# Kernel tuning notes

Hardware: AMD Instinct MI355X
Metric: run time of the kernel (lower is better)

Reference implementation:

```python
import jax, jax.numpy as jnp
import numpy as np

QMIN, QMAX = -128, 127  # int8 range


def _quantize(x, scale, zero_point):
    """Affine quantize float -> int8: clamp(round(x/scale) + zp, -128, 127)."""
    q = jnp.round(x / scale) + zero_point
    return jnp.clip(q, QMIN, QMAX).astype(jnp.int8)


def setup_inputs() -> dict:
    key = jax.random.key(0)
    k1, k2, k3 = jax.random.split(key, 3)
    N, IN, OUT = 8192, 4096, 4096
    inp = jax.random.normal(k1, (N, IN), dtype=jnp.float32)
    # int8 weight table [OUT, IN]
    weight = jax.random.randint(k2, (OUT, IN), QMIN, QMAX + 1, dtype=jnp.int32).astype(jnp.int8)
    # int32 bias [OUT]
    bias = jax.random.randint(k3, (OUT,), -(2 ** 15), 2 ** 15, dtype=jnp.int32)
    return {
        "input": inp,
        "weight": weight,
        "bias": bias,
        "input_scale": 0.02,
        "input_zero_point": 0,
        "output_scale": 4096.0,
        "output_zero_point": 0,
    }


def reference(input, weight, bias, input_scale, input_zero_point, output_scale, output_zero_point):
    # 1) affine quantize input to int8
    q_input = _quantize(input, input_scale, input_zero_point)
    # 2) int32 matmul: F.linear(q_input.int32, weight.int32, bias.int32)
    acc = jnp.matmul(q_input.astype(jnp.int32), weight.astype(jnp.int32).T) + bias  # [N, OUT] int32
    # 3) requantize int32 accumulator to int8 with output scale/zero-point
    q_output = _quantize(acc.astype(jnp.float32), output_scale, output_zero_point)
    return q_output
```

## Files before the change

### kernel.cpp

```cpp
#include <hip/hip_runtime.h>
#include <stdint.h>

typedef int v4i __attribute__((ext_vector_type(4)));
typedef int v16i __attribute__((ext_vector_type(16)));

__device__ __forceinline__ int clamp_i8(int v) {
    return v < -128 ? -128 : (v > 127 ? 127 : v);
}

__device__ __forceinline__ void async_load16(const void* g, void* l) {
    __builtin_amdgcn_global_load_lds(
        (const __attribute__((address_space(1))) void*)g,
        (__attribute__((address_space(3))) void*)l, 16, 0, 0);
}

__global__ void quant_input_kernel(const float* __restrict__ x, int8_t* __restrict__ q,
                                   const float* __restrict__ scale_p,
                                   const int* __restrict__ zp_p, int n4) {
    int t = blockIdx.x * blockDim.x + threadIdx.x;
    if (t >= n4) return;
    const float inv = 1.0f / *scale_p;
    const int zp = *zp_p;
    float4 v = ((const float4*)x)[t];
    int q0 = clamp_i8((int)rintf(v.x * inv) + zp);
    int q1 = clamp_i8((int)rintf(v.y * inv) + zp);
    int q2 = clamp_i8((int)rintf(v.z * inv) + zp);
    int q3 = clamp_i8((int)rintf(v.w * inv) + zp);
    int packed = (q0 & 255) | ((q1 & 255) << 8) | ((q2 & 255) << 16) | ((q3 & 255) << 24);
    ((int*)q)[t] = packed;
}

__global__ void pack_weight_kernel(const int* __restrict__ w, int8_t* __restrict__ q, int n4) {
    int t = blockIdx.x * blockDim.x + threadIdx.x;
    if (t >= n4) return;
    int4 v = ((const int4*)w)[t];
    int packed = (v.x & 255) | ((v.y & 255) << 8) | ((v.z & 255) << 16) | ((v.w & 255) << 24);
    ((int*)q)[t] = packed;
}

#define BM 256
#define BN 128
#define BK 64

__global__ __launch_bounds__(256, 2) void gemm_i8_kernel(
    const int8_t* __restrict__ A, const int8_t* __restrict__ W,
    const int* __restrict__ bias, int* __restrict__ C,
    const float* __restrict__ oscale_p, const int* __restrict__ ozp_p,
    int N, int K, int M) {
    __shared__ int8_t lA[BM * BK];
    __shared__ int8_t lB[BN * BK];

    const int tid = threadIdx.x;
    const int lane = tid & 63;
    const int w = tid >> 6;
    const int wm = w >> 1;
    const int wn = w & 1;

    const int bm = blockIdx.y * BM;
    const int bn = blockIdx.x * BN;

    const int s_sub = lane >> 2;
    const int s_col = (((lane & 3) ^ ((s_sub >> 1) & 3))) * 16;
    const int8_t* gA = A + (int64_t)(bm + w * 64 + s_sub) * K + s_col;
    const int8_t* gB = W + (int64_t)(bn + w * 32 + s_sub) * K + s_col;
    int8_t* lA0 = &lA[w * 4096];
    int8_t* lB0 = &lB[w * 2048];
    const int64_t rs = (int64_t)16 * K;

    const int m0 = lane & 31;
    const int rsw = (m0 >> 1) & 3;
    const int chi = lane >> 5;

    v16i acc[4][2];
#pragma unroll
    for (int i = 0; i < 4; i++)
#pragma unroll
        for (int j = 0; j < 2; j++)
#pragma unroll
            for (int r = 0; r < 16; r++) acc[i][j][r] = 0;

    for (int kt = 0; kt < K; kt += BK) {
        async_load16(gA, lA0);
        async_load16(gA + rs, lA0 + 1024);
        async_load16(gA + 2 * rs, lA0 + 2048);
        async_load16(gA + 3 * rs, lA0 + 3072);
        async_load16(gB, lB0);
        async_load16(gB + rs, lB0 + 1024);
        gA += BK;
        gB += BK;
        __syncthreads();

#pragma unroll
        for (int k0 = 0; k0 < BK; k0 += 32) {
            const int cb = k0 >> 4;
            v4i af[4], bf[2];
#pragma unroll
            for (int ms = 0; ms < 4; ms++)
                af[ms] = *(const v4i*)&lA[(wm * 128 + ms * 32 + m0) * BK +
                                          (((cb + chi) ^ rsw) << 4)];
#pragma unroll
            for (int ns = 0; ns < 2; ns++)
                bf[ns] = *(const v4i*)&lB[(wn * 64 + ns * 32 + m0) * BK +
                                          (((cb + chi) ^ rsw) << 4)];

#pragma unroll
            for (int ms = 0; ms < 4; ms++)
#pragma unroll
                for (int ns = 0; ns < 2; ns++)
                    acc[ms][ns] = __builtin_amdgcn_mfma_i32_32x32x32_i8(
                        af[ms], bf[ns], acc[ms][ns], 0, 0, 0);
        }
        __syncthreads();
    }

    const float inv_os = 1.0f / *oscale_p;
    const int ozp = *ozp_p;
    const int rbase = 4 * (lane >> 5);
#pragma unroll
    for (int ns = 0; ns < 2; ns++) {
        const int gn = bn + wn * 64 + ns * 32 + m0;
        const int bv = bias[gn];
#pragma unroll
        for (int ms = 0; ms < 4; ms++) {
            const int gm0 = bm + wm * 128 + ms * 32 + rbase;
            v16i a = acc[ms][ns];
#pragma unroll
            for (int reg = 0; reg < 16; reg++) {
                const int row = (reg & 3) + 8 * (reg >> 2);
                int v = a[reg] + bv;
                int q = (int)rintf((float)v * inv_os) + ozp;
                q = clamp_i8(q);
                C[(int64_t)(gm0 + row) * M + gn] = q;
            }
        }
    }
}

extern "C" void kernel_launch(void* const* d_in, const int* in_sizes, int n_in,
                              void* d_out, int out_size, void* d_ws, size_t ws_size,
                              hipStream_t stream) {
    const float* x = (const float*)d_in[0];
    const int* wgt = (const int*)d_in[1];
    const int* bias = (const int*)d_in[2];
    const float* in_scale = (const float*)d_in[3];
    const int* in_zp = (const int*)d_in[4];
    const float* out_scale = (const float*)d_in[5];
    const int* out_zp = (const int*)d_in[6];

    const int64_t x_elems = (int64_t)in_sizes[0];
    const int OUT = in_sizes[2];
    const int K = in_sizes[1] / OUT;
    const int N = (int)(x_elems / K);

    int8_t* qA = (int8_t*)d_ws;
    int8_t* qW = qA + x_elems;

    {
        int n4 = (int)(x_elems / 4);
        quant_input_kernel<<<(n4 + 255) / 256, 256, 0, stream>>>(x, qA, in_scale, in_zp, n4);
    }
    {
        int n4 = (int)(((int64_t)OUT * K) / 4);
        pack_weight_kernel<<<(n4 + 255) / 256, 256, 0, stream>>>(wgt, qW, n4);
    }
    dim3 grid(OUT / BN, N / BM);
    gemm_i8_kernel<<<grid, 256, 0, stream>>>(qA, qW, bias, (int*)d_out,
                                             out_scale, out_zp, N, K, OUT);
}
```

Before: 424.5 us.

## Double-buffer LDS tiles in int8 GEMM and widen prepass kernels to 16 elements

The GEMM main loop now keeps two LDS buffers for A and B. It prefetches the next K tile with async global-to-LDS loads while MFMAs run on the current tile, which drops one barrier per iteration. The quantize and weight-pack prepass kernels now handle 16 elements per thread and write 16-byte stores instead of 4-byte ones. Doubling LDS to 48KB per block cuts the headroom for occupancy. The overlap only helps if the wait that the barrier inserts does not serialize the prefetch.

Result: no change. 420.0 us (-1.1%).

```diff
diff --git a/kernel.cpp b/kernel.cpp
--- a/kernel.cpp
+++ b/kernel.cpp
@@ -14,28 +14,38 @@
         (__attribute__((address_space(3))) void*)l, 16, 0, 0);
 }
 
-__global__ void quant_input_kernel(const float* __restrict__ x, int8_t* __restrict__ q,
+__global__ void quant_input_kernel(const float4* __restrict__ x, int4* __restrict__ q,
                                    const float* __restrict__ scale_p,
-                                   const int* __restrict__ zp_p, int n4) {
+                                   const int* __restrict__ zp_p, int n16) {
     int t = blockIdx.x * blockDim.x + threadIdx.x;
-    if (t >= n4) return;
+    if (t >= n16) return;
     const float inv = 1.0f / *scale_p;
     const int zp = *zp_p;
-    float4 v = ((const float4*)x)[t];
-    int q0 = clamp_i8((int)rintf(v.x * inv) + zp);
-    int q1 = clamp_i8((int)rintf(v.y * inv) + zp);
-    int q2 = clamp_i8((int)rintf(v.z * inv) + zp);
-    int q3 = clamp_i8((int)rintf(v.w * inv) + zp);
-    int packed = (q0 & 255) | ((q1 & 255) << 8) | ((q2 & 255) << 16) | ((q3 & 255) << 24);
-    ((int*)q)[t] = packed;
-}
-
-__global__ void pack_weight_kernel(const int* __restrict__ w, int8_t* __restrict__ q, int n4) {
+    int4 out;
+    int* op = (int*)&out;
+#pragma unroll
+    for (int j = 0; j < 4; j++) {
+        float4 v = x[4 * t + j];
+        int q0 = clamp_i8((int)rintf(v.x * inv) + zp);
+        int q1 = clamp_i8((int)rintf(v.y * inv) + zp);
+        int q2 = clamp_i8((int)rintf(v.z * inv) + zp);
+        int q3 = clamp_i8((int)rintf(v.w * inv) + zp);
+        op[j] = (q0 & 255) | ((q1 & 255) << 8) | ((q2 & 255) << 16) | ((q3 & 255) << 24);
+    }
+    q[t] = out;
+}
+
+__global__ void pack_weight_kernel(const int4* __restrict__ w, int4* __restrict__ q, int n16) {
     int t = blockIdx.x * blockDim.x + threadIdx.x;
-    if (t >= n4) return;
-    int4 v = ((const int4*)w)[t];
-    int packed = (v.x & 255) | ((v.y & 255) << 8) | ((v.z & 255) << 16) | ((v.w & 255) << 24);
-    ((int*)q)[t] = packed;
+    if (t >= n16) return;
+    int4 out;
+    int* op = (int*)&out;
+#pragma unroll
+    for (int j = 0; j < 4; j++) {
+        int4 v = w[4 * t + j];
+        op[j] = (v.x & 255) | ((v.y & 255) << 8) | ((v.z & 255) << 16) | ((v.w & 255) << 24);
+    }
+    q[t] = out;
 }
 
 #define BM 256
@@ -47,8 +57,8 @@
     const int* __restrict__ bias, int* __restrict__ C,
     const float* __restrict__ oscale_p, const int* __restrict__ ozp_p,
     int N, int K, int M) {
-    __shared__ int8_t lA[BM * BK];
-    __shared__ int8_t lB[BN * BK];
+    __shared__ int8_t lA[2][BM * BK];
+    __shared__ int8_t lB[2][BN * BK];
 
     const int tid = threadIdx.x;
     const int lane = tid & 63;
@@ -63,9 +73,11 @@
     const int s_col = (((lane & 3) ^ ((s_sub >> 1) & 3))) * 16;
     const int8_t* gA = A + (int64_t)(bm + w * 64 + s_sub) * K + s_col;
     const int8_t* gB = W + (int64_t)(bn + w * 32 + s_sub) * K + s_col;
-    int8_t* lA0 = &lA[w * 4096];
-    int8_t* lB0 = &lB[w * 2048];
     const int64_t rs = (int64_t)16 * K;
+    int8_t* lA0 = &lA[0][w * 4096];
+    int8_t* lA1 = &lA[1][w * 4096];
+    int8_t* lB0 = &lB[0][w * 2048];
+    int8_t* lB1 = &lB[1][w * 2048];
 
     const int m0 = lane & 31;
     const int rsw = (m0 >> 1) & 3;
@@ -79,7 +91,7 @@
 #pragma unroll
             for (int r = 0; r < 16; r++) acc[i][j][r] = 0;
 
-    for (int kt = 0; kt < K; kt += BK) {
+    {
         async_load16(gA, lA0);
         async_load16(gA + rs, lA0 + 1024);
         async_load16(gA + 2 * rs, lA0 + 2048);
@@ -88,19 +100,36 @@
         async_load16(gB + rs, lB0 + 1024);
         gA += BK;
         gB += BK;
+    }
+
+    int cur = 0;
+    for (int kt = 0; kt < K; kt += BK) {
         __syncthreads();
-
+        if (kt + BK < K) {
+            int8_t* dA = cur ? lA0 : lA1;
+            int8_t* dB = cur ? lB0 : lB1;
+            async_load16(gA, dA);
+            async_load16(gA + rs, dA + 1024);
+            async_load16(gA + 2 * rs, dA + 2048);
+            async_load16(gA + 3 * rs, dA + 3072);
+            async_load16(gB, dB);
+            async_load16(gB + rs, dB + 1024);
+            gA += BK;
+            gB += BK;
+        }
+        const int8_t* cA = &lA[cur][0];
+        const int8_t* cB = &lB[cur][0];
 #pragma unroll
         for (int k0 = 0; k0 < BK; k0 += 32) {
             const int cb = k0 >> 4;
             v4i af[4], bf[2];
 #pragma unroll
             for (int ms = 0; ms < 4; ms++)
-                af[ms] = *(const v4i*)&lA[(wm * 128 + ms * 32 + m0) * BK +
+                af[ms] = *(const v4i*)&cA[(wm * 128 + ms * 32 + m0) * BK +
                                           (((cb + chi) ^ rsw) << 4)];
 #pragma unroll
             for (int ns = 0; ns < 2; ns++)
-                bf[ns] = *(const v4i*)&lB[(wn * 64 + ns * 32 + m0) * BK +
+                bf[ns] = *(const v4i*)&cB[(wn * 64 + ns * 32 + m0) * BK +
                                           (((cb + chi) ^ rsw) << 4)];
 
 #pragma unroll
@@ -110,7 +139,7 @@
                     acc[ms][ns] = __builtin_amdgcn_mfma_i32_32x32x32_i8(
                         af[ms], bf[ns], acc[ms][ns], 0, 0, 0);
         }
-        __syncthreads();
+        cur ^= 1;
     }
 
     const float inv_os = 1.0f / *oscale_p;
@@ -156,12 +185,14 @@
     int8_t* qW = qA + x_elems;
 
     {
-        int n4 = (int)(x_elems / 4);
-        quant_input_kernel<<<(n4 + 255) / 256, 256, 0, stream>>>(x, qA, in_scale, in_zp, n4);
+        int n16 = (int)(x_elems / 16);
+        quant_input_kernel<<<(n16 + 255) / 256, 256, 0, stream>>>(
+            (const float4*)x, (int4*)qA, in_scale, in_zp, n16);
     }
     {
-        int n4 = (int)(((int64_t)OUT * K) / 4);
-        pack_weight_kernel<<<(n4 + 255) / 256, 256, 0, stream>>>(wgt, qW, n4);
+        int n16 = (int)(((int64_t)OUT * K) / 16);
+        pack_weight_kernel<<<(n16 + 255) / 256, 256, 0, stream>>>(
+            (const int4*)wgt, (int4*)qW, n16);
     }
     dim3 grid(OUT / BN, N / BM);
     gemm_i8_kernel<<<grid, 256, 0, stream>>>(qA, qW, bias, (int*)d_out,
```
